# Kernel optimization log

Hardware: AMD Instinct MI355X
Metric: run time of the kernel (lower is better)

The kernel has to match this reference:

```python
import jax, jax.numpy as jnp
import numpy as np

N_SKU, N_WH, N_SUP = 100000, 5000, 2000
D_IN, D_OUT, H = 128, 64, 4
DH = D_OUT // H  # 16
E_INTRA, E_CROSS = 400000, 200000
EPS_LN = 1e-5


def setup_inputs() -> dict:
    key = jax.random.key(0)
    ks = jax.random.split(key, 40)
    f32 = jnp.float32

    def edges(k, E, n_src, n_dst):
        k1, k2 = jax.random.split(k)
        return jnp.stack([
            jax.random.randint(k1, (E,), 0, n_src),
            jax.random.randint(k2, (E,), 0, n_dst),
        ]).astype(jnp.int32)

    inp = {
        'x_sku': jax.random.normal(ks[0], (N_SKU, D_IN), f32),
        'x_wh': jax.random.normal(ks[1], (N_WH, D_IN), f32),
        'x_sup': jax.random.normal(ks[2], (N_SUP, D_IN), f32),
    }
    names = ['plant', 'pg', 'sg', 'st', 'ship', 'supply']
    for i, nm in enumerate(names):
        inp['W_' + nm] = jax.random.normal(ks[3 + 2 * i], (D_IN, D_OUT), f32) * 0.05
        inp['a_' + nm] = jax.random.normal(ks[4 + 2 * i], (2 * DH,), f32) * 0.05
    inp['proj_W'] = jax.random.normal(ks[20], (2 * D_OUT, D_OUT), f32) * 0.05
    inp['proj_b'] = jnp.zeros((D_OUT,), f32)
    inp['ln_g'] = jnp.ones((D_OUT,), f32)
    inp['ln_b'] = jnp.zeros((D_OUT,), f32)
    inp['res_W'] = jax.random.normal(ks[21], (D_IN, D_OUT), f32) * 0.05
    inp['ei_plant'] = edges(ks[22], E_INTRA, N_SKU, N_SKU)
    inp['ei_pg'] = edges(ks[23], E_INTRA, N_SKU, N_SKU)
    inp['ei_sg'] = edges(ks[24], E_INTRA, N_SKU, N_SKU)
    inp['ei_st'] = edges(ks[25], E_INTRA, N_SKU, N_SKU)
    inp['ei_ship'] = edges(ks[26], E_CROSS, N_SKU, N_WH)
    inp['ei_supply'] = edges(ks[27], E_CROSS, N_SKU, N_SUP)
    return inp


def _gat_conv(src_feat, dst_feat, ei, W, a, num_dst):
    """One-edge-type multi-head GAT: ELU edge scores, per-dst softmax, scatter-add."""
    src_i, dst_i = ei[0], ei[1]
    h_src = (src_feat @ W).reshape(-1, H, DH)  # [N_src, H, dh]
    h_dst = (dst_feat @ W).reshape(-1, H, DH)  # [N_dst, H, dh]
    hs = h_src[src_i]  # [E, H, dh] gather
    hd = h_dst[dst_i]  # [E, H, dh]
    # a^T [h_src || h_dst], shared attention vector across heads
    e = jax.nn.elu(hs @ a[:DH] + hd @ a[DH:])  # [E, H]
    # numerically stable scatter-softmax over edges grouped by dst node
    e_max = jax.lax.stop_gradient(jax.ops.segment_max(e, dst_i, num_segments=num_dst))
    e_max = jnp.where(jnp.isfinite(e_max), e_max, 0.0)
    exp_e = jnp.exp(e - e_max[dst_i])
    denom = jax.ops.segment_sum(exp_e, dst_i, num_segments=num_dst)
    alpha = exp_e / (denom[dst_i] + 1e-12)  # [E, H]
    out = jax.ops.segment_sum(alpha[..., None] * hs, dst_i, num_segments=num_dst)
    return out.reshape(num_dst, D_OUT)


def reference(x_sku, x_wh, x_sup,
              W_plant, a_plant, W_pg, a_pg, W_sg, a_sg, W_st, a_st,
              W_ship, a_ship, W_supply, a_supply,
              proj_W, proj_b, ln_g, ln_b, res_W,
              ei_plant, ei_pg, ei_sg, ei_st, ei_ship, ei_supply):
    # branch A (intra sku->sku edge types), summed into sku accumulator
    oa_sku = (_gat_conv(x_sku, x_sku, ei_plant, W_plant, a_plant, N_SKU)
              + _gat_conv(x_sku, x_sku, ei_pg, W_pg, a_pg, N_SKU)
              + _gat_conv(x_sku, x_sku, ei_sg, W_sg, a_sg, N_SKU)
              + _gat_conv(x_sku, x_sku, ei_st, W_st, a_st, N_SKU))
    ob_sku = jnp.zeros((N_SKU, D_OUT), x_sku.dtype)
    # branch B (cross edge types)
    oa_wh = jnp.zeros((N_WH, D_OUT), x_wh.dtype)
    ob_wh = _gat_conv(x_sku, x_wh, ei_ship, W_ship, a_ship, N_WH)
    oa_sup = jnp.zeros((N_SUP, D_OUT), x_sup.dtype)
    ob_sup = _gat_conv(x_sku, x_sup, ei_supply, W_supply, a_supply, N_SUP)

    def finish(x, oa, ob):
        y = jnp.concatenate([oa, ob], axis=-1) @ proj_W + proj_b + x @ res_W
        mu = y.mean(-1, keepdims=True)
        var = ((y - mu) ** 2).mean(-1, keepdims=True)
        return (y - mu) / jnp.sqrt(var + EPS_LN) * ln_g + ln_b

    return (finish(x_sku, oa_sku, ob_sku),
            finish(x_wh, oa_wh, ob_wh),
            finish(x_sup, oa_sup, ob_sup))
```

## Files before the change

kernel.cpp:

```cpp
#include <hip/hip_runtime.h>
#include <hip/hip_bf16.h>
#include <cstdint>

#define NS 100000
#define NW 5000
#define NPS 2000
#define DI 128
#define DO 64
#define NSTRIPS (NS/16)
#define NFLAT (4*NS + NW + NPS)
#define NWPAD 5008
#define NBUK 134
#define BCAP 20480
#define CHUNK 8192

typedef unsigned short bfu;
typedef __attribute__((ext_vector_type(8))) short s8v;
typedef __attribute__((ext_vector_type(4))) float f4v;

__device__ inline bfu f2bf(float f) {
  uint32_t u = __float_as_uint(f);
  u = (u + 0x7FFFu + ((u >> 16) & 1u)) >> 16;
  return (bfu)u;
}
__device__ inline float bf2f(bfu u) {
  return __uint_as_float((uint32_t)u << 16);
}

__global__ void k_convert3(const float* __restrict__ x0, bfu* __restrict__ o0, int n0,
                           const float* __restrict__ x1, bfu* __restrict__ o1, int n1,
                           const float* __restrict__ x2, bfu* __restrict__ o2, int n2) {
  int t = blockIdx.x * 256 + threadIdx.x;
  const float* x; bfu* o; int i;
  if (t < n0) { x = x0; o = o0; i = t; }
  else if (t < n0 + n1) { x = x1; o = o1; i = t - n0; }
  else if (t < n0 + n1 + n2) { x = x2; o = o2; i = t - n0 - n1; }
  else return;
  const float4* p = (const float4*)x + (size_t)i * 2;
  float4 a = p[0], b = p[1];
  uint4 v;
  v.x = (uint32_t)f2bf(a.x) | ((uint32_t)f2bf(a.y) << 16);
  v.y = (uint32_t)f2bf(a.z) | ((uint32_t)f2bf(a.w) << 16);
  v.z = (uint32_t)f2bf(b.x) | ((uint32_t)f2bf(b.y) << 16);
  v.w = (uint32_t)f2bf(b.z) | ((uint32_t)f2bf(b.w) << 16);
  ((uint4*)o)[i] = v;
}

struct PackArgs {
  const float* W[6]; const float* a[6];
  const float* resW; const float* projW;
  bfu* Bp; bfu* Rp; bfu* Pp;
  float* wv_wh; float* wv_sup;
};
__global__ void k_pack_all(PackArgs P) {
  int t = blockIdx.x * 256 + threadIdx.x;
  if (t < 61440) {
    int ty = t / 10240, rem = t % 10240;
    int r = rem / 128, k = rem % 128;
    const float* W = P.W[ty]; const float* a = P.a[ty];
    float v = 0.f;
    if (r < 64) v = W[k * 64 + r];
    else if (r < 72) {
      int h = (r - 64) & 3;
      const float* av = (r < 68) ? a : (a + 16);
      #pragma unroll
      for (int m = 0; m < 16; ++m) v += W[k * 64 + h * 16 + m] * av[m];
    }
    P.Bp[ty * 10240 + rem] = f2bf(v);
  } else if (t < 69632) {
    int i = t - 61440; int j = i / 128, k = i % 128;
    P.Rp[i] = f2bf(P.resW[k * 64 + j]);
  } else if (t < 77824) {
    int i = t - 69632; int j = i / 128, k = i % 128;
    P.Pp[i] = f2bf(P.projW[k * 64 + j]);
  } else if (t < 78848) {
    int i = t - 77824; int which = i / 512;
    int k = (i % 512) / 4, h = i % 4;
    const float* W = P.W[4 + which]; const float* a = P.a[4 + which];
    float v = 0.f;
    #pragma unroll
    for (int m = 0; m < 16; ++m) v += W[k * 64 + h * 16 + m] * a[16 + m];
    (which ? P.wv_sup : P.wv_wh)[k * 4 + h] = v;
  }
}

__global__ __launch_bounds__(256, 2) void k_gemm2t(const bfu* __restrict__ xb,
    const bfu* __restrict__ Bp0, const bfu* __restrict__ Bp1,
    bfu* __restrict__ hb0, bfu* __restrict__ hb1,
    float* __restrict__ ss0, float* __restrict__ ss1,
    float* __restrict__ sd0, float* __restrict__ sd1, int nstrips) {
  int lane = threadIdx.x & 63;
  int l15 = lane & 15, q = lane >> 4;
  int w  = (int)((blockIdx.x * blockDim.x + threadIdx.x) >> 6);
  int nw = (int)((gridDim.x * blockDim.x) >> 6);
  s8v bfr[10][4];
  #pragma unroll
  for (int nt = 0; nt < 5; ++nt)
    #pragma unroll
    for (int kq = 0; kq < 4; ++kq) {
      bfr[nt][kq]     = *(const s8v*)(Bp0 + (size_t)(nt * 16 + l15) * 128 + kq * 32 + q * 8);
      bfr[5 + nt][kq] = *(const s8v*)(Bp1 + (size_t)(nt * 16 + l15) * 128 + kq * 32 + q * 8);
    }
  for (int s = w; s < nstrips; s += nw) {
    int mb = s * 16;
    f4v acc[10];
    #pragma unroll
    for (int u = 0; u < 10; ++u) acc[u] = (f4v){0.f, 0.f, 0.f, 0.f};
    const bfu* ar = xb + (size_t)(mb + l15) * 128 + q * 8;
    #pragma unroll
    for (int kq = 0; kq < 4; ++kq) {
      s8v af = *(const s8v*)(ar + kq * 32);
      #pragma unroll
      for (int u = 0; u < 10; ++u)
        acc[u] = __builtin_amdgcn_mfma_f32_16x16x32_bf16(af, bfr[u][kq], acc[u], 0, 0, 0);
    }
    #pragma unroll
    for (int u = 0; u < 10; ++u) {
      int nt = (u < 5) ? u : u - 5;
      bfu* hb = (u < 5) ? hb0 : hb1;
      float* ssrc = (u < 5) ? ss0 : ss1;
      float* sdst = (u < 5) ? sd0 : sd1;
      int c = nt * 16 + l15;
      #pragma unroll
      for (int r = 0; r < 4; ++r) {
        int node = mb + q * 4 + r;
        float v = acc[u][r];
        if (c < 64)      hb[(size_t)node * 64 + c] = f2bf(v);
        else if (c < 68) ssrc[(size_t)node * 4 + (c - 64)] = v;
        else if (c < 72) sdst[(size_t)node * 4 + (c - 68)] = v;
      }
    }
  }
}

__global__ __launch_bounds__(256) void k_scores(const float* __restrict__ x,
    const float* __restrict__ wv, float* __restrict__ sdst, int N) {
  int lane = threadIdx.x & 63;
  int w  = (int)((blockIdx.x * 256 + threadIdx.x) >> 6);
  int nw = (int)((gridDim.x * 256) >> 6);
  float4 wa = ((const float4*)wv)[lane];
  float4 wb = ((const float4*)wv)[64 + lane];
  for (int n = w; n < N; n += nw) {
    float xa = x[(size_t)n * 128 + lane], xc = x[(size_t)n * 128 + 64 + lane];
    float4 a;
    a.x = xa * wa.x + xc * wb.x; a.y = xa * wa.y + xc * wb.y;
    a.z = xa * wa.z + xc * wb.z; a.w = xa * wa.w + xc * wb.w;
    #pragma unroll
    for (int m = 1; m < 64; m <<= 1) {
      a.x += __shfl_xor(a.x, m); a.y += __shfl_xor(a.y, m);
      a.z += __shfl_xor(a.z, m); a.w += __shfl_xor(a.w, m);
    }
    if (lane == 0) ((float4*)sdst)[n] = a;
  }
}

struct ESeg { const int* ei[6]; int E[6]; int Ecum[7]; };

__device__ inline void buk_of(int t, int d, int& b, int& loc) {
  if (t < 4)       { int f = d * 4 + t; b = f >> 12;        loc = f & 4095; }
  else if (t == 4) { b = 98 + (d >> 8);                     loc = d & 255; }
  else             { b = 118 + (d >> 7);                    loc = d & 127; }
}

__global__ void k_init_cur(int* __restrict__ gCur) {
  int t = threadIdx.x;
  if (t < NBUK) gCur[t] = t * BCAP;
}

__global__ __launch_bounds__(256) void k_bin(ESeg S, int* __restrict__ gCur,
                                             uint32_t* __restrict__ binned, int ETOT) {
  __shared__ int cnt[NBUK];
  __shared__ int runb[NBUK];
  int tid = threadIdx.x;
  int gbase = blockIdx.x * CHUNK;
  if (tid < NBUK) cnt[tid] = 0;
  __syncthreads();
  #pragma unroll 4
  for (int i = 0; i < CHUNK / 256; ++i) {
    int g = gbase + i * 256 + tid;
    if (g < ETOT) {
      int t = 0;
      #pragma unroll
      for (int k = 0; k < 5; ++k) t += (g >= S.Ecum[k + 1]);
      int e = g - S.Ecum[t];
      int d = S.ei[t][S.E[t] + e];
      int b, loc; buk_of(t, d, b, loc);
      atomicAdd(&cnt[b], 1);
    }
  }
  __syncthreads();
  if (tid < NBUK) { runb[tid] = atomicAdd(&gCur[tid], cnt[tid]); cnt[tid] = 0; }
  __syncthreads();
  #pragma unroll 4
  for (int i = 0; i < CHUNK / 256; ++i) {
    int g = gbase + i * 256 + tid;
    if (g < ETOT) {
      int t = 0;
      #pragma unroll
      for (int k = 0; k < 5; ++k) t += (g >= S.Ecum[k + 1]);
      int e = g - S.Ecum[t];
      int sv = S.ei[t][e];
      int d  = S.ei[t][S.E[t] + e];
      int b, loc; buk_of(t, d, b, loc);
      int pos = runb[b] + atomicAdd(&cnt[b], 1);
      if (pos < (b + 1) * BCAP)
        binned[pos] = ((uint32_t)loc << 17) | (uint32_t)sv;
    }
  }
}

__global__ __launch_bounds__(1024) void k_csr(const int* __restrict__ gCur,
    const uint32_t* __restrict__ binned, int* __restrict__ offs,
    int* __restrict__ ssorted) {
  __shared__ int hist[4096];
  __shared__ int wsc[16];
  __shared__ int bbase_s, cnt_s;
  int b = blockIdx.x, tid = threadIdx.x;
  int lane = tid & 63, wid = tid >> 6;
  if (tid == 0) {
    int bb = 0, own = 0;
    for (int k = 0; k < NBUK; ++k) {
      int c = min(gCur[k] - k * BCAP, BCAP);
      if (k < b) bb += c;
      if (k == b) own = c;
    }
    bbase_s = bb; cnt_s = own;
  }
  #pragma unroll
  for (int k = 0; k < 4; ++k) hist[tid * 4 + k] = 0;
  __syncthreads();
  int cnt = cnt_s, bbase = bbase_s;
  const uint32_t* bk = binned + (size_t)b * BCAP;
  for (int i = tid; i < cnt; i += 1024)
    atomicAdd(&hist[bk[i] >> 17], 1);
  __syncthreads();
  int t4 = tid * 4;
  int v0 = hist[t4], v1 = hist[t4 + 1], v2 = hist[t4 + 2], v3 = hist[t4 + 3];
  int tsum = v0 + v1 + v2 + v3;
  int inc = tsum;
  #pragma unroll
  for (int d = 1; d < 64; d <<= 1) { int tt = __shfl_up(inc, d); if (lane >= d) inc += tt; }
  if (lane == 63) wsc[wid] = inc;
  __syncthreads();
  int wpre = 0;
  for (int k = 0; k < wid; ++k) wpre += wsc[k];
  int excl = inc - tsum + wpre;
  hist[t4] = excl;
  hist[t4 + 1] = excl + v0;
  hist[t4 + 2] = excl + v0 + v1;
  hist[t4 + 3] = excl + v0 + v1 + v2;
  __syncthreads();
  int sbase, nslots;
  if (b < 98)        { sbase = b << 12;                nslots = min(4096, 4 * NS - sbase); }
  else if (b < 118)  { int lb = (b - 98) << 8;  sbase = 4 * NS + lb;      nslots = min(256, NW - lb); }
  else               { int lb = (b - 118) << 7; sbase = 4 * NS + NW + lb; nslots = min(128, NPS - lb); }
  for (int i = tid; i < nslots; i += 1024) offs[sbase + i] = bbase + hist[i];
  if (b == NBUK - 1 && tid == 0) offs[NFLAT] = bbase + cnt;
  __syncthreads();
  for (int i = tid; i < cnt; i += 1024) {
    uint32_t v = bk[i];
    int p = atomicAdd(&hist[v >> 17], 1);
    ssorted[bbase + p] = (int)(v & 0x1FFFFu);
  }
}

struct AggArgs {
  const int* offs; const int* srcs;
  const bfu* hbAll;
  const float* ssAll;
  const float* sdAll;
  const float* sd_wh; const float* sd_sup;
  bfu* osku; bfu* owh; bfu* osup;
};

__global__ __launch_bounds__(256) void k_megaagg(AggArgs A) {
  int lane = threadIdx.x & 63;
  int q = lane >> 4, m = lane & 15, h = m >> 2;
  int qsh = q << 4;
  int w  = (int)((blockIdx.x * 256 + threadIdx.x) >> 6);
  int nw = (int)((gridDim.x * 256) >> 6);
  for (int n = w; n < NS + NW + NPS; n += nw) {
    if (n < NS) {
      const int* ob = A.offs + (size_t)n * 4;
      int4 o = *(const int4*)ob;
      int o4 = ob[4];
      int sb = (q == 0) ? o.x : (q == 1) ? o.y : (q == 2) ? o.z : o.w;
      int se = (q == 0) ? o.y : (q == 1) ? o.z : (q == 2) ? o.w : o4;
      int len = se - sb;
      int maxlen = max(max(o.y - o.x, o.z - o.y), max(o.w - o.z, o4 - o.w));
      float sdv = A.sdAll[((size_t)q * NS + n) * 4 + h];
      uint32_t tbase = (uint32_t)q * (uint32_t)NS;
      float den = 0.f, a0 = 0.f, a1 = 0.f, a2 = 0.f, a3 = 0.f;
      for (int j0 = 0; j0 < maxlen; j0 += 16) {
        int ei = j0 + m;
        int sidx = (ei < len) ? A.srcs[sb + ei] : 0;
        int gmax = min(16, maxlen - j0);
        for (int jj = 0; jj < gmax; jj += 8) {
          float sc[8]; uint2 hv[8]; int vj[8];
          #pragma unroll
          for (int i = 0; i < 8; ++i) {
            int j = jj + i;
            int s = __shfl(sidx, qsh + j);
            vj[i] = (j0 + j) < len;
            uint32_t nb = tbase + (uint32_t)s;
            sc[i] = A.ssAll[nb * 4u + (uint32_t)h];
            hv[i] = *(const uint2*)(A.hbAll + nb * 64u + (uint32_t)(m * 4));
          }
          #pragma unroll
          for (int i = 0; i < 8; ++i) {
            float e = sc[i] + sdv;
            e = e > 0.f ? e : (__expf(e) - 1.f);
            float wgt = vj[i] ? __expf(e) : 0.f;
            den += wgt;
            a0 = fmaf(__uint_as_float(hv[i].x << 16), wgt, a0);
            a1 = fmaf(__uint_as_float(hv[i].x & 0xffff0000u), wgt, a1);
            a2 = fmaf(__uint_as_float(hv[i].y << 16), wgt, a2);
            a3 = fmaf(__uint_as_float(hv[i].y & 0xffff0000u), wgt, a3);
          }
        }
      }
      float inv = __builtin_amdgcn_rcpf(den + 1e-12f);
      float r0 = a0 * inv, r1 = a1 * inv, r2 = a2 * inv, r3 = a3 * inv;
      r0 += __shfl_xor(r0, 16); r0 += __shfl_xor(r0, 32);
      r1 += __shfl_xor(r1, 16); r1 += __shfl_xor(r1, 32);
      r2 += __shfl_xor(r2, 16); r2 += __shfl_xor(r2, 32);
      r3 += __shfl_xor(r3, 16); r3 += __shfl_xor(r3, 32);
      if (q == 0) {
        uint2 pk;
        pk.x = (uint32_t)f2bf(r0) | ((uint32_t)f2bf(r1) << 16);
        pk.y = (uint32_t)f2bf(r2) | ((uint32_t)f2bf(r3) << 16);
        *(uint2*)(A.osku + (size_t)n * 64 + m * 4) = pk;
      }
    } else {
      int tt, nl; const float* sd; bfu* op;
      int fi;
      if (n < NS + NW) { tt = 4; nl = n - NS; fi = 4 * NS + nl; sd = A.sd_wh; op = A.owh + (size_t)nl * 64; }
      else { tt = 5; nl = n - NS - NW; fi = 4 * NS + NW + nl; sd = A.sd_sup; op = A.osup + (size_t)nl * 64; }
      int beg = A.offs[fi], end = A.offs[fi + 1];
      uint32_t tbase = (uint32_t)tt * (uint32_t)NS;
      float sdv = sd[(size_t)nl * 4 + h];
      float den = 0.f, a0 = 0.f, a1 = 0.f, a2 = 0.f, a3 = 0.f;
      for (int cb = beg; cb < end; cb += 64) {
        int rem = min(64, end - cb);
        int sidx = (lane < rem) ? A.srcs[cb + lane] : 0;
        for (int jb = 0; jb < rem; jb += 32) {
          float sc[8]; uint2 hv[8]; int vj[8];
          #pragma unroll
          for (int i = 0; i < 8; ++i) {
            int eidx = jb + 4 * i + q;
            int s = __shfl(sidx, eidx);
            vj[i] = eidx < rem;
            uint32_t nb = tbase + (uint32_t)s;
            sc[i] = A.ssAll[nb * 4u + (uint32_t)h];
            hv[i] = *(const uint2*)(A.hbAll + nb * 64u + (uint32_t)(m * 4));
          }
          #pragma unroll
          for (int i = 0; i < 8; ++i) {
            float e = sc[i] + sdv;
            e = e > 0.f ? e : (__expf(e) - 1.f);
            float wgt = vj[i] ? __expf(e) : 0.f;
            den += wgt;
            a0 = fmaf(__uint_as_float(hv[i].x << 16), wgt, a0);
            a1 = fmaf(__uint_as_float(hv[i].x & 0xffff0000u), wgt, a1);
            a2 = fmaf(__uint_as_float(hv[i].y << 16), wgt, a2);
            a3 = fmaf(__uint_as_float(hv[i].y & 0xffff0000u), wgt, a3);
          }
        }
      }
      den += __shfl_xor(den, 16); den += __shfl_xor(den, 32);
      a0 += __shfl_xor(a0, 16); a0 += __shfl_xor(a0, 32);
      a1 += __shfl_xor(a1, 16); a1 += __shfl_xor(a1, 32);
      a2 += __shfl_xor(a2, 16); a2 += __shfl_xor(a2, 32);
      a3 += __shfl_xor(a3, 16); a3 += __shfl_xor(a3, 32);
      float inv = __builtin_amdgcn_rcpf(den + 1e-12f);
      if (q == 0) {
        uint2 pk;
        pk.x = (uint32_t)f2bf(a0 * inv) | ((uint32_t)f2bf(a1 * inv) << 16);
        pk.y = (uint32_t)f2bf(a2 * inv) | ((uint32_t)f2bf(a3 * inv) << 16);
        *(uint2*)(op + m * 4) = pk;
      }
    }
  }
}

__global__ __launch_bounds__(256) void k_finishM(const bfu* __restrict__ aggb,
    const bfu* __restrict__ xbf, const bfu* __restrict__ Pp, int koff,
    const bfu* __restrict__ Rp, const float* __restrict__ pb,
    const float* __restrict__ g, const float* __restrict__ bb,
    float* __restrict__ outp, int N, int nstrips) {
  int lane = threadIdx.x & 63, l15 = lane & 15, q = lane >> 4;
  int w  = (int)((blockIdx.x * 256 + threadIdx.x) >> 6);
  int nw = (int)((gridDim.x * 256) >> 6);
  s8v bP[4][2], bR[4][4];
  float pbv[4], gv[4], bv[4];
  #pragma unroll
  for (int c = 0; c < 4; ++c) {
    const bfu* pr = Pp + (size_t)(c * 16 + l15) * 128 + koff;
    bP[c][0] = *(const s8v*)(pr + q * 8);
    bP[c][1] = *(const s8v*)(pr + 32 + q * 8);
    const bfu* rr = Rp + (size_t)(c * 16 + l15) * 128;
    #pragma unroll
    for (int kq = 0; kq < 4; ++kq) bR[c][kq] = *(const s8v*)(rr + kq * 32 + q * 8);
    pbv[c] = pb[c * 16 + l15]; gv[c] = g[c * 16 + l15]; bv[c] = bb[c * 16 + l15];
  }
  for (int s = w; s < nstrips; s += nw) {
    int mb = s * 16;
    const bfu* ar = aggb + (size_t)(mb + l15) * 64 + q * 8;
    const bfu* xr = xbf + (size_t)(mb + l15) * 128 + q * 8;
    s8v a0 = *(const s8v*)ar, a1 = *(const s8v*)(ar + 32);
    s8v x0 = *(const s8v*)xr, x1 = *(const s8v*)(xr + 32),
        x2 = *(const s8v*)(xr + 64), x3 = *(const s8v*)(xr + 96);
    f4v acc[4];
    #pragma unroll
    for (int c = 0; c < 4; ++c) {
      acc[c] = (f4v){0.f, 0.f, 0.f, 0.f};
      acc[c] = __builtin_amdgcn_mfma_f32_16x16x32_bf16(a0, bP[c][0], acc[c], 0, 0, 0);
      acc[c] = __builtin_amdgcn_mfma_f32_16x16x32_bf16(a1, bP[c][1], acc[c], 0, 0, 0);
      acc[c] = __builtin_amdgcn_mfma_f32_16x16x32_bf16(x0, bR[c][0], acc[c], 0, 0, 0);
      acc[c] = __builtin_amdgcn_mfma_f32_16x16x32_bf16(x1, bR[c][1], acc[c], 0, 0, 0);
      acc[c] = __builtin_amdgcn_mfma_f32_16x16x32_bf16(x2, bR[c][2], acc[c], 0, 0, 0);
      acc[c] = __builtin_amdgcn_mfma_f32_16x16x32_bf16(x3, bR[c][3], acc[c], 0, 0, 0);
    }
    #pragma unroll
    for (int r = 0; r < 4; ++r) {
      int row = mb + q * 4 + r;
      float y0 = acc[0][r] + pbv[0], y1 = acc[1][r] + pbv[1];
      float y2 = acc[2][r] + pbv[2], y3 = acc[3][r] + pbv[3];
      float s1 = y0 + y1 + y2 + y3;
      s1 += __shfl_xor(s1, 1); s1 += __shfl_xor(s1, 2);
      s1 += __shfl_xor(s1, 4); s1 += __shfl_xor(s1, 8);
      float mu = s1 * 0.015625f;
      float d0 = y0 - mu, d1 = y1 - mu, d2 = y2 - mu, d3 = y3 - mu;
      float s2 = d0 * d0 + d1 * d1 + d2 * d2 + d3 * d3;
      s2 += __shfl_xor(s2, 1); s2 += __shfl_xor(s2, 2);
      s2 += __shfl_xor(s2, 4); s2 += __shfl_xor(s2, 8);
      float rs = rsqrtf(s2 * 0.015625f + 1e-5f);
      if (row < N) {
        float* orow = outp + (size_t)row * 64 + l15;
        orow[0]  = d0 * rs * gv[0] + bv[0];
        orow[16] = d1 * rs * gv[1] + bv[1];
        orow[32] = d2 * rs * gv[2] + bv[2];
        orow[48] = d3 * rs * gv[3] + bv[3];
      }
    }
  }
}

extern "C" void kernel_launch(void* const* d_in, const int* in_sizes, int n_in,
                              void* d_out, int out_size, void* d_ws, size_t ws_size,
                              hipStream_t stream) {
  const float* x_sku = (const float*)d_in[0];
  const float* x_wh  = (const float*)d_in[1];
  const float* x_sup = (const float*)d_in[2];
  const float* Wt[6]; const float* at[6];
  for (int t = 0; t < 6; ++t) { Wt[t] = (const float*)d_in[3 + 2 * t]; at[t] = (const float*)d_in[4 + 2 * t]; }
  const float* projW = (const float*)d_in[15];
  const float* projb = (const float*)d_in[16];
  const float* lng   = (const float*)d_in[17];
  const float* lnb   = (const float*)d_in[18];
  const float* resW  = (const float*)d_in[19];
  const int* ei[6]; int Et[6];
  for (int t = 0; t < 6; ++t) { ei[t] = (const int*)d_in[20 + t]; Et[t] = in_sizes[20 + t] / 2; }
  float* out = (float*)d_out;

  int ETOT = 0;
  for (int t = 0; t < 6; ++t) ETOT += Et[t];

  char* ws = (char*)d_ws;
  size_t off = 0;
  auto alloc = [&](size_t bytes) { off = (off + 255) & ~(size_t)255; void* p = ws + off; off += bytes; return p; };

  bfu*  xb      = (bfu*)alloc((size_t)NS * DI * 2);
  bfu*  xb_wh   = (bfu*)alloc((size_t)NWPAD * DI * 2);
  bfu*  xb_sup  = (bfu*)alloc((size_t)NPS * DI * 2);
  bfu*  Bp      = (bfu*)alloc((size_t)6 * 80 * 128 * 2);
  bfu*  Rp      = (bfu*)alloc((size_t)64 * 128 * 2);
  bfu*  Pp      = (bfu*)alloc((size_t)64 * 128 * 2);
  float* wv_wh  = (float*)alloc(128 * 4 * 4);
  float* wv_sup = (float*)alloc(128 * 4 * 4);
  bfu*  hbAll   = (bfu*)alloc((size_t)6 * NS * 64 * 2);
  float* ssAll  = (float*)alloc((size_t)6 * NS * 4 * 4);
  float* sdAll  = (float*)alloc((size_t)6 * NS * 4 * 4);
  float* sdst_wh  = (float*)alloc((size_t)NW * 4 * 4);
  float* sdst_sup = (float*)alloc((size_t)NPS * 4 * 4);
  size_t agg_bytes = ((size_t)NS + NWPAD + NPS) * 64 * 2;
  size_t bin_bytes = (size_t)NBUK * BCAP * 4;
  char* un = (char*)alloc(agg_bytes > bin_bytes ? agg_bytes : bin_bytes);
  bfu* agg_sku = (bfu*)un;
  bfu* agg_wh  = agg_sku + (size_t)NS * 64;
  bfu* agg_sup = agg_wh + (size_t)NWPAD * 64;
  uint32_t* binned = (uint32_t*)un;
  int* gCur    = (int*)alloc(256 * 4);
  int* offsb   = (int*)alloc((size_t)(NFLAT + 1) * 4);
  int* ssorted = (int*)alloc((size_t)ETOT * 4);

  int n0 = NS * 16, n1 = NW * 16, n2 = NPS * 16;
  k_convert3<<<(n0 + n1 + n2 + 255) / 256, 256, 0, stream>>>(x_sku, xb, n0, x_wh, xb_wh, n1,
                                                             x_sup, xb_sup, n2);

  PackArgs PA;
  for (int t = 0; t < 6; ++t) { PA.W[t] = Wt[t]; PA.a[t] = at[t]; }
  PA.resW = resW; PA.projW = projW; PA.Bp = Bp; PA.Rp = Rp; PA.Pp = Pp;
  PA.wv_wh = wv_wh; PA.wv_sup = wv_sup;
  k_pack_all<<<(78848 + 255) / 256, 256, 0, stream>>>(PA);

  k_scores<<<1250, 256, 0, stream>>>(x_wh, wv_wh, sdst_wh, NW);
  k_scores<<<500, 256, 0, stream>>>(x_sup, wv_sup, sdst_sup, NPS);

  ESeg S;
  S.Ecum[0] = 0;
  for (int t = 0; t < 6; ++t) { S.ei[t] = ei[t]; S.E[t] = Et[t]; S.Ecum[t + 1] = S.Ecum[t] + Et[t]; }
  k_init_cur<<<1, 256, 0, stream>>>(gCur);
  k_bin<<<(ETOT + CHUNK - 1) / CHUNK, 256, 0, stream>>>(S, gCur, binned, ETOT);
  k_csr<<<NBUK, 1024, 0, stream>>>(gCur, binned, offsb, ssorted);

  for (int p = 0; p < 3; ++p) {
    int t0 = 2 * p, t1 = 2 * p + 1;
    k_gemm2t<<<512, 256, 0, stream>>>(xb, Bp + (size_t)t0 * 10240, Bp + (size_t)t1 * 10240,
        hbAll + (size_t)t0 * NS * 64, hbAll + (size_t)t1 * NS * 64,
        ssAll + (size_t)t0 * NS * 4, ssAll + (size_t)t1 * NS * 4,
        sdAll + (size_t)t0 * NS * 4, sdAll + (size_t)t1 * NS * 4, NSTRIPS);
  }

  AggArgs A;
  A.offs = offsb; A.srcs = ssorted;
  A.hbAll = hbAll; A.ssAll = ssAll; A.sdAll = sdAll;
  A.sd_wh = sdst_wh; A.sd_sup = sdst_sup;
  A.osku = agg_sku; A.owh = agg_wh; A.osup = agg_sup;
  k_megaagg<<<(NS + NW + NPS + 3) / 4, 256, 0, stream>>>(A);

  k_finishM<<<1563, 256, 0, stream>>>(agg_sku, xb, Pp, 0, Rp, projb, lng, lnb, out, NS, NSTRIPS);
  k_finishM<<<79, 256, 0, stream>>>(agg_wh, xb_wh, Pp, 64, Rp, projb, lng, lnb,
                                    out + (size_t)NS * 64, NW, NWPAD / 16);
  k_finishM<<<32, 256, 0, stream>>>(agg_sup, xb_sup, Pp, 64, Rp, projb, lng, lnb,
                                    out + (size_t)(NS + NW) * 64, NPS, NPS / 16);
}
```

Measured before the change: 416.1 us.

## Merge front-end, GEMM and finish launches into fewer multi-role kernels

Folds the convert, pack, scores, init and bin kernels into one block-role-dispatched front kernel, the three GEMM launches into one 1536-block grid, and the three finish launches into one. The scores kernel now computes its attention-weight vectors inline instead of reading a precomputed buffer, and bin cursors become per-bucket local offsets cleared with a memset. The aim is to cut launch overhead and inter-kernel gaps by letting independent stages run concurrently. The cost is extra per-block dispatch logic and shared-memory use sized for the largest role in the merged kernel.

```diff
diff --git a/kernel.cpp b/kernel.cpp
--- a/kernel.cpp
+++ b/kernel.cpp
@@ -14,6 +14,11 @@
 #define BCAP 20480
 #define CHUNK 8192
 
+#define B_CONV 6688
+#define B_PACK 304
+#define B_SWH  157
+#define B_SSUP 63
+
 typedef unsigned short bfu;
 typedef __attribute__((ext_vector_type(8))) short s8v;
 typedef __attribute__((ext_vector_type(4))) float f4v;
@@ -27,14 +32,77 @@
   return __uint_as_float((uint32_t)u << 16);
 }
 
-__global__ void k_convert3(const float* __restrict__ x0, bfu* __restrict__ o0, int n0,
-                           const float* __restrict__ x1, bfu* __restrict__ o1, int n1,
-                           const float* __restrict__ x2, bfu* __restrict__ o2, int n2) {
-  int t = blockIdx.x * 256 + threadIdx.x;
+struct ESeg { const int* ei[6]; int E[6]; int Ecum[7]; };
+
+__device__ inline void buk_of(int t, int d, int& b, int& loc) {
+  if (t < 4)       { int f = d * 4 + t; b = f >> 12;        loc = f & 4095; }
+  else if (t == 4) { b = 98 + (d >> 8);                     loc = d & 255; }
+  else             { b = 118 + (d >> 7);                    loc = d & 127; }
+}
+
+struct PackA {
+  const float* W[6]; const float* a[6];
+  const float* resW; const float* projW;
+  bfu* Bp; bfu* Rp; bfu* Pp;
+};
+
+struct K1Args {
+  ESeg S; int* gCur; uint32_t* binned; int ETOT; int nbin;
+  const float* x0; bfu* o0; int n0;
+  const float* x1; bfu* o1; int n1;
+  const float* x2; bfu* o2; int n2;
+  PackA P;
+  const float* xwh; const float* xsup; float* sd_wh; float* sd_sup;
+};
+
+__device__ void bin_body(const K1Args& A, int bid) {
+  __shared__ int cnt[NBUK];
+  __shared__ int runb[NBUK];
+  const ESeg& S = A.S;
+  int tid = threadIdx.x;
+  int gbase = bid * CHUNK;
+  if (tid < NBUK) cnt[tid] = 0;
+  __syncthreads();
+  #pragma unroll 4
+  for (int i = 0; i < CHUNK / 256; ++i) {
+    int g = gbase + i * 256 + tid;
+    if (g < A.ETOT) {
+      int t = 0;
+      #pragma unroll
+      for (int k = 0; k < 5; ++k) t += (g >= S.Ecum[k + 1]);
+      int e = g - S.Ecum[t];
+      int d = S.ei[t][S.E[t] + e];
+      int b, loc; buk_of(t, d, b, loc);
+      atomicAdd(&cnt[b], 1);
+    }
+  }
+  __syncthreads();
+  if (tid < NBUK) { runb[tid] = atomicAdd(&A.gCur[tid], cnt[tid]); cnt[tid] = 0; }
+  __syncthreads();
+  #pragma unroll 4
+  for (int i = 0; i < CHUNK / 256; ++i) {
+    int g = gbase + i * 256 + tid;
+    if (g < A.ETOT) {
+      int t = 0;
+      #pragma unroll
+      for (int k = 0; k < 5; ++k) t += (g >= S.Ecum[k + 1]);
+      int e = g - S.Ecum[t];
+      int sv = S.ei[t][e];
+      int d  = S.ei[t][S.E[t] + e];
+      int b, loc; buk_of(t, d, b, loc);
+      int pos = runb[b] + atomicAdd(&cnt[b], 1);
+      if (pos < BCAP)
+        A.binned[(size_t)b * BCAP + pos] = ((uint32_t)loc << 17) | (uint32_t)sv;
+    }
+  }
+}
+
+__device__ void convert_body(const K1Args& A, int bid) {
+  int t = bid * 256 + threadIdx.x;
   const float* x; bfu* o; int i;
-  if (t < n0) { x = x0; o = o0; i = t; }
-  else if (t < n0 + n1) { x = x1; o = o1; i = t - n0; }
-  else if (t < n0 + n1 + n2) { x = x2; o = o2; i = t - n0 - n1; }
+  if (t < A.n0) { x = A.x0; o = A.o0; i = t; }
+  else if (t < A.n0 + A.n1) { x = A.x1; o = A.o1; i = t - A.n0; }
+  else if (t < A.n0 + A.n1 + A.n2) { x = A.x2; o = A.o2; i = t - A.n0 - A.n1; }
   else return;
   const float4* p = (const float4*)x + (size_t)i * 2;
   float4 a = p[0], b = p[1];
@@ -46,14 +114,8 @@
   ((uint4*)o)[i] = v;
 }
 
-struct PackArgs {
-  const float* W[6]; const float* a[6];
-  const float* resW; const float* projW;
-  bfu* Bp; bfu* Rp; bfu* Pp;
-  float* wv_wh; float* wv_sup;
-};
-__global__ void k_pack_all(PackArgs P) {
-  int t = blockIdx.x * 256 + threadIdx.x;
+__device__ void pack_body(const PackA& P, int bid) {
+  int t = bid * 256 + threadIdx.x;
   if (t < 61440) {
     int ty = t / 10240, rem = t % 10240;
     int r = rem / 128, k = rem % 128;
@@ -73,26 +135,126 @@
   } else if (t < 77824) {
     int i = t - 69632; int j = i / 128, k = i % 128;
     P.Pp[i] = f2bf(P.projW[k * 64 + j]);
-  } else if (t < 78848) {
-    int i = t - 77824; int which = i / 512;
-    int k = (i % 512) / 4, h = i % 4;
-    const float* W = P.W[4 + which]; const float* a = P.a[4 + which];
-    float v = 0.f;
-    #pragma unroll
-    for (int m = 0; m < 16; ++m) v += W[k * 64 + h * 16 + m] * a[16 + m];
-    (which ? P.wv_sup : P.wv_wh)[k * 4 + h] = v;
-  }
-}
-
-__global__ __launch_bounds__(256, 2) void k_gemm2t(const bfu* __restrict__ xb,
-    const bfu* __restrict__ Bp0, const bfu* __restrict__ Bp1,
-    bfu* __restrict__ hb0, bfu* __restrict__ hb1,
-    float* __restrict__ ss0, float* __restrict__ ss1,
-    float* __restrict__ sd0, float* __restrict__ sd1, int nstrips) {
+  }
+}
+
+__device__ void scores_body(const float* __restrict__ x, const float* __restrict__ W,
+                            const float* __restrict__ a, float* __restrict__ sdst,
+                            int N, int bid, int nblk) {
+  int tid = threadIdx.x;
+  int lane = tid & 63;
+  float wa[4] = {0.f, 0.f, 0.f, 0.f}, wb[4] = {0.f, 0.f, 0.f, 0.f};
+  for (int m = 0; m < 16; ++m) {
+    float av = a[16 + m];
+    #pragma unroll
+    for (int h = 0; h < 4; ++h) {
+      wa[h] += W[lane * 64 + h * 16 + m] * av;
+      wb[h] += W[(64 + lane) * 64 + h * 16 + m] * av;
+    }
+  }
+  int w  = (bid * 256 + tid) >> 6;
+  int nw = (nblk * 256) >> 6;
+  for (int n = w; n < N; n += nw) {
+    float xa = x[(size_t)n * 128 + lane], xc = x[(size_t)n * 128 + 64 + lane];
+    float4 r;
+    r.x = xa * wa[0] + xc * wb[0]; r.y = xa * wa[1] + xc * wb[1];
+    r.z = xa * wa[2] + xc * wb[2]; r.w = xa * wa[3] + xc * wb[3];
+    #pragma unroll
+    for (int m = 1; m < 64; m <<= 1) {
+      r.x += __shfl_xor(r.x, m); r.y += __shfl_xor(r.y, m);
+      r.z += __shfl_xor(r.z, m); r.w += __shfl_xor(r.w, m);
+    }
+    if (lane == 0) ((float4*)sdst)[n] = r;
+  }
+}
+
+__global__ __launch_bounds__(256) void k_front(K1Args A) {
+  int bid = blockIdx.x;
+  if (bid < A.nbin) { bin_body(A, bid); return; }
+  bid -= A.nbin;
+  if (bid < B_CONV) { convert_body(A, bid); return; }
+  bid -= B_CONV;
+  if (bid < B_PACK) { pack_body(A.P, bid); return; }
+  bid -= B_PACK;
+  if (bid < B_SWH) { scores_body(A.xwh, A.P.W[4], A.P.a[4], A.sd_wh, NW, bid, B_SWH); return; }
+  bid -= B_SWH;
+  scores_body(A.xsup, A.P.W[5], A.P.a[5], A.sd_sup, NPS, bid, B_SSUP);
+}
+
+__global__ __launch_bounds__(1024) void k_csr(const int* __restrict__ gCur,
+    const uint32_t* __restrict__ binned, int* __restrict__ offs,
+    int* __restrict__ ssorted) {
+  __shared__ int hist[4096];
+  __shared__ int wsc[16];
+  __shared__ int bbase_s, cnt_s;
+  int b = blockIdx.x, tid = threadIdx.x;
+  int lane = tid & 63, wid = tid >> 6;
+  if (tid == 0) {
+    int bb = 0, own = 0;
+    for (int k = 0; k < NBUK; ++k) {
+      int c = min(gCur[k], BCAP);
+      if (k < b) bb += c;
+      if (k == b) own = c;
+    }
+    bbase_s = bb; cnt_s = own;
+  }
+  #pragma unroll
+  for (int k = 0; k < 4; ++k) hist[tid * 4 + k] = 0;
+  __syncthreads();
+  int cnt = cnt_s, bbase = bbase_s;
+  const uint32_t* bk = binned + (size_t)b * BCAP;
+  for (int i = tid; i < cnt; i += 1024)
+    atomicAdd(&hist[bk[i] >> 17], 1);
+  __syncthreads();
+  int t4 = tid * 4;
+  int v0 = hist[t4], v1 = hist[t4 + 1], v2 = hist[t4 + 2], v3 = hist[t4 + 3];
+  int tsum = v0 + v1 + v2 + v3;
+  int inc = tsum;
+  #pragma unroll
+  for (int d = 1; d < 64; d <<= 1) { int tt = __shfl_up(inc, d); if (lane >= d) inc += tt; }
+  if (lane == 63) wsc[wid] = inc;
+  __syncthreads();
+  int wpre = 0;
+  for (int k = 0; k < wid; ++k) wpre += wsc[k];
+  int excl = inc - tsum + wpre;
+  hist[t4] = excl;
+  hist[t4 + 1] = excl + v0;
+  hist[t4 + 2] = excl + v0 + v1;
+  hist[t4 + 3] = excl + v0 + v1 + v2;
+  __syncthreads();
+  int sbase, nslots;
+  if (b < 98)        { sbase = b << 12;                nslots = min(4096, 4 * NS - sbase); }
+  else if (b < 118)  { int lb = (b - 98) << 8;  sbase = 4 * NS + lb;      nslots = min(256, NW - lb); }
+  else               { int lb = (b - 118) << 7; sbase = 4 * NS + NW + lb; nslots = min(128, NPS - lb); }
+  for (int i = tid; i < nslots; i += 1024) offs[sbase + i] = bbase + hist[i];
+  if (b == NBUK - 1 && tid == 0) offs[NFLAT] = bbase + cnt;
+  __syncthreads();
+  for (int i = tid; i < cnt; i += 1024) {
+    uint32_t v = bk[i];
+    int p = atomicAdd(&hist[v >> 17], 1);
+    ssorted[bbase + p] = (int)(v & 0x1FFFFu);
+  }
+}
+
+struct GemmArgs {
+  const bfu* xb; const bfu* Bp;
+  bfu* hbAll; float* ssAll; float* sdAll; int nstrips;
+};
+__global__ __launch_bounds__(256, 2) void k_gemm(GemmArgs G) {
+  int p = blockIdx.x >> 9;
+  int bloc = blockIdx.x & 511;
+  const bfu* Bp0 = G.Bp + (size_t)(2 * p) * 10240;
+  const bfu* Bp1 = G.Bp + (size_t)(2 * p + 1) * 10240;
+  bfu* hb0 = G.hbAll + (size_t)(2 * p) * NS * 64;
+  bfu* hb1 = G.hbAll + (size_t)(2 * p + 1) * NS * 64;
+  float* ss0 = G.ssAll + (size_t)(2 * p) * NS * 4;
+  float* ss1 = G.ssAll + (size_t)(2 * p + 1) * NS * 4;
+  float* sd0 = G.sdAll + (size_t)(2 * p) * NS * 4;
+  float* sd1 = G.sdAll + (size_t)(2 * p + 1) * NS * 4;
   int lane = threadIdx.x & 63;
   int l15 = lane & 15, q = lane >> 4;
-  int w  = (int)((blockIdx.x * blockDim.x + threadIdx.x) >> 6);
-  int nw = (int)((gridDim.x * blockDim.x) >> 6);
+  int w  = (int)((bloc * 256 + threadIdx.x) >> 6);
+  int nw = (512 * 256) >> 6;
   s8v bfr[10][4];
   #pragma unroll
   for (int nt = 0; nt < 5; ++nt)
@@ -101,12 +263,12 @@
       bfr[nt][kq]     = *(const s8v*)(Bp0 + (size_t)(nt * 16 + l15) * 128 + kq * 32 + q * 8);
       bfr[5 + nt][kq] = *(const s8v*)(Bp1 + (size_t)(nt * 16 + l15) * 128 + kq * 32 + q * 8);
     }
-  for (int s = w; s < nstrips; s += nw) {
+  for (int s = w; s < G.nstrips; s += nw) {
     int mb = s * 16;
     f4v acc[10];
     #pragma unroll
     for (int u = 0; u < 10; ++u) acc[u] = (f4v){0.f, 0.f, 0.f, 0.f};
-    const bfu* ar = xb + (size_t)(mb + l15) * 128 + q * 8;
+    const bfu* ar = G.xb + (size_t)(mb + l15) * 128 + q * 8;
     #pragma unroll
     for (int kq = 0; kq < 4; ++kq) {
       s8v af = *(const s8v*)(ar + kq * 32);
@@ -130,137 +292,6 @@
         else if (c < 72) sdst[(size_t)node * 4 + (c - 68)] = v;
       }
     }
-  }
-}
-
-__global__ __launch_bounds__(256) void k_scores(const float* __restrict__ x,
-    const float* __restrict__ wv, float* __restrict__ sdst, int N) {
-  int lane = threadIdx.x & 63;
-  int w  = (int)((blockIdx.x * 256 + threadIdx.x) >> 6);
-  int nw = (int)((gridDim.x * 256) >> 6);
-  float4 wa = ((const float4*)wv)[lane];
-  float4 wb = ((const float4*)wv)[64 + lane];
-  for (int n = w; n < N; n += nw) {
-    float xa = x[(size_t)n * 128 + lane], xc = x[(size_t)n * 128 + 64 + lane];
-    float4 a;
-    a.x = xa * wa.x + xc * wb.x; a.y = xa * wa.y + xc * wb.y;
-    a.z = xa * wa.z + xc * wb.z; a.w = xa * wa.w + xc * wb.w;
-    #pragma unroll
-    for (int m = 1; m < 64; m <<= 1) {
-      a.x += __shfl_xor(a.x, m); a.y += __shfl_xor(a.y, m);
-      a.z += __shfl_xor(a.z, m); a.w += __shfl_xor(a.w, m);
-    }
-    if (lane == 0) ((float4*)sdst)[n] = a;
-  }
-}
-
-struct ESeg { const int* ei[6]; int E[6]; int Ecum[7]; };
-
-__device__ inline void buk_of(int t, int d, int& b, int& loc) {
-  if (t < 4)       { int f = d * 4 + t; b = f >> 12;        loc = f & 4095; }
-  else if (t == 4) { b = 98 + (d >> 8);                     loc = d & 255; }
-  else             { b = 118 + (d >> 7);                    loc = d & 127; }
-}
-
-__global__ void k_init_cur(int* __restrict__ gCur) {
-  int t = threadIdx.x;
-  if (t < NBUK) gCur[t] = t * BCAP;
-}
-
-__global__ __launch_bounds__(256) void k_bin(ESeg S, int* __restrict__ gCur,
-                                             uint32_t* __restrict__ binned, int ETOT) {
-  __shared__ int cnt[NBUK];
-  __shared__ int runb[NBUK];
-  int tid = threadIdx.x;
-  int gbase = blockIdx.x * CHUNK;
-  if (tid < NBUK) cnt[tid] = 0;
-  __syncthreads();
-  #pragma unroll 4
-  for (int i = 0; i < CHUNK / 256; ++i) {
-    int g = gbase + i * 256 + tid;
-    if (g < ETOT) {
-      int t = 0;
-      #pragma unroll
-      for (int k = 0; k < 5; ++k) t += (g >= S.Ecum[k + 1]);
-      int e = g - S.Ecum[t];
-      int d = S.ei[t][S.E[t] + e];
-      int b, loc; buk_of(t, d, b, loc);
-      atomicAdd(&cnt[b], 1);
-    }
-  }
-  __syncthreads();
-  if (tid < NBUK) { runb[tid] = atomicAdd(&gCur[tid], cnt[tid]); cnt[tid] = 0; }
-  __syncthreads();
-  #pragma unroll 4
-  for (int i = 0; i < CHUNK / 256; ++i) {
-    int g = gbase + i * 256 + tid;
-    if (g < ETOT) {
-      int t = 0;
-      #pragma unroll
-      for (int k = 0; k < 5; ++k) t += (g >= S.Ecum[k + 1]);
-      int e = g - S.Ecum[t];
-      int sv = S.ei[t][e];
-      int d  = S.ei[t][S.E[t] + e];
-      int b, loc; buk_of(t, d, b, loc);
-      int pos = runb[b] + atomicAdd(&cnt[b], 1);
-      if (pos < (b + 1) * BCAP)
-        binned[pos] = ((uint32_t)loc << 17) | (uint32_t)sv;
-    }
-  }
-}
-
-__global__ __launch_bounds__(1024) void k_csr(const int* __restrict__ gCur,
-    const uint32_t* __restrict__ binned, int* __restrict__ offs,
-    int* __restrict__ ssorted) {
-  __shared__ int hist[4096];
-  __shared__ int wsc[16];
-  __shared__ int bbase_s, cnt_s;
-  int b = blockIdx.x, tid = threadIdx.x;
-  int lane = tid & 63, wid = tid >> 6;
-  if (tid == 0) {
-    int bb = 0, own = 0;
-    for (int k = 0; k < NBUK; ++k) {
-      int c = min(gCur[k] - k * BCAP, BCAP);
-      if (k < b) bb += c;
-      if (k == b) own = c;
-    }
-    bbase_s = bb; cnt_s = own;
-  }
-  #pragma unroll
-  for (int k = 0; k < 4; ++k) hist[tid * 4 + k] = 0;
-  __syncthreads();
-  int cnt = cnt_s, bbase = bbase_s;
-  const uint32_t* bk = binned + (size_t)b * BCAP;
-  for (int i = tid; i < cnt; i += 1024)
-    atomicAdd(&hist[bk[i] >> 17], 1);
-  __syncthreads();
-  int t4 = tid * 4;
-  int v0 = hist[t4], v1 = hist[t4 + 1], v2 = hist[t4 + 2], v3 = hist[t4 + 3];
-  int tsum = v0 + v1 + v2 + v3;
-  int inc = tsum;
-  #pragma unroll
-  for (int d = 1; d < 64; d <<= 1) { int tt = __shfl_up(inc, d); if (lane >= d) inc += tt; }
-  if (lane == 63) wsc[wid] = inc;
-  __syncthreads();
-  int wpre = 0;
-  for (int k = 0; k < wid; ++k) wpre += wsc[k];
-  int excl = inc - tsum + wpre;
-  hist[t4] = excl;
-  hist[t4 + 1] = excl + v0;
-  hist[t4 + 2] = excl + v0 + v1;
-  hist[t4 + 3] = excl + v0 + v1 + v2;
-  __syncthreads();
-  int sbase, nslots;
-  if (b < 98)        { sbase = b << 12;                nslots = min(4096, 4 * NS - sbase); }
-  else if (b < 118)  { int lb = (b - 98) << 8;  sbase = 4 * NS + lb;      nslots = min(256, NW - lb); }
-  else               { int lb = (b - 118) << 7; sbase = 4 * NS + NW + lb; nslots = min(128, NPS - lb); }
-  for (int i = tid; i < nslots; i += 1024) offs[sbase + i] = bbase + hist[i];
-  if (b == NBUK - 1 && tid == 0) offs[NFLAT] = bbase + cnt;
-  __syncthreads();
-  for (int i = tid; i < cnt; i += 1024) {
-    uint32_t v = bk[i];
-    int p = atomicAdd(&hist[v >> 17], 1);
-    ssorted[bbase + p] = (int)(v & 0x1FFFFu);
   }
 }
 
@@ -383,25 +414,42 @@
   }
 }
 
-__global__ __launch_bounds__(256) void k_finishM(const bfu* __restrict__ aggb,
-    const bfu* __restrict__ xbf, const bfu* __restrict__ Pp, int koff,
-    const bfu* __restrict__ Rp, const float* __restrict__ pb,
-    const float* __restrict__ g, const float* __restrict__ bb,
-    float* __restrict__ outp, int N, int nstrips) {
+struct FinArgs {
+  const bfu* agg0; const bfu* agg1; const bfu* agg2;
+  const bfu* x0; const bfu* x1; const bfu* x2;
+  float* out0; float* out1; float* out2;
+  const bfu* Pp; const bfu* Rp;
+  const float* pb; const float* g; const float* bb;
+  int bcut0, bcut1;
+};
+
+__global__ __launch_bounds__(256) void k_finish(FinArgs F) {
+  int bid = blockIdx.x;
+  int role = (bid >= F.bcut0) + (bid >= F.bcut1);
+  int b0 = (role == 0) ? 0 : (role == 1) ? F.bcut0 : F.bcut1;
+  int nb = (role == 0) ? F.bcut0 : (role == 1) ? (F.bcut1 - F.bcut0) : ((int)gridDim.x - F.bcut1);
+  int bloc = bid - b0;
+  const bfu* aggb = (role == 0) ? F.agg0 : (role == 1) ? F.agg1 : F.agg2;
+  const bfu* xbf  = (role == 0) ? F.x0 : (role == 1) ? F.x1 : F.x2;
+  float* outp     = (role == 0) ? F.out0 : (role == 1) ? F.out1 : F.out2;
+  int koff    = (role == 0) ? 0 : 64;
+  int N       = (role == 0) ? NS : (role == 1) ? NW : NPS;
+  int nstrips = (role == 0) ? NSTRIPS : (role == 1) ? (NWPAD / 16) : (NPS / 16);
+
   int lane = threadIdx.x & 63, l15 = lane & 15, q = lane >> 4;
-  int w  = (int)((blockIdx.x * 256 + threadIdx.x) >> 6);
-  int nw = (int)((gridDim.x * 256) >> 6);
+  int w  = (int)((bloc * 256 + threadIdx.x) >> 6);
+  int nw = nb << 2;
   s8v bP[4][2], bR[4][4];
   float pbv[4], gv[4], bv[4];
   #pragma unroll
   for (int c = 0; c < 4; ++c) {
-    const bfu* pr = Pp + (size_t)(c * 16 + l15) * 128 + koff;
+    const bfu* pr = F.Pp + (size_t)(c * 16 + l15) * 128 + koff;
     bP[c][0] = *(const s8v*)(pr + q * 8);
     bP[c][1] = *(const s8v*)(pr + 32 + q * 8);
-    const bfu* rr = Rp + (size_t)(c * 16 + l15) * 128;
+    const bfu* rr = F.Rp + (size_t)(c * 16 + l15) * 128;
     #pragma unroll
     for (int kq = 0; kq < 4; ++kq) bR[c][kq] = *(const s8v*)(rr + kq * 32 + q * 8);
-    pbv[c] = pb[c * 16 + l15]; gv[c] = g[c * 16 + l15]; bv[c] = bb[c * 16 + l15];
+    pbv[c] = F.pb[c * 16 + l15]; gv[c] = F.g[c * 16 + l15]; bv[c] = F.bb[c * 16 + l15];
   }
   for (int s = w; s < nstrips; s += nw) {
     int mb = s * 16;
@@ -476,8 +524,6 @@
   bfu*  Bp      = (bfu*)alloc((size_t)6 * 80 * 128 * 2);
   bfu*  Rp      = (bfu*)alloc((size_t)64 * 128 * 2);
   bfu*  Pp      = (bfu*)alloc((size_t)64 * 128 * 2);
-  float* wv_wh  = (float*)alloc(128 * 4 * 4);
-  float* wv_sup = (float*)alloc(128 * 4 * 4);
   bfu*  hbAll   = (bfu*)alloc((size_t)6 * NS * 64 * 2);
   float* ssAll  = (float*)alloc((size_t)6 * NS * 4 * 4);
   float* sdAll  = (float*)alloc((size_t)6 * NS * 4 * 4);
@@ -494,33 +540,27 @@
   int* offsb   = (int*)alloc((size_t)(NFLAT + 1) * 4);
   int* ssorted = (int*)alloc((size_t)ETOT * 4);
 
-  int n0 = NS * 16, n1 = NW * 16, n2 = NPS * 16;
-  k_convert3<<<(n0 + n1 + n2 + 255) / 256, 256, 0, stream>>>(x_sku, xb, n0, x_wh, xb_wh, n1,
-                                                             x_sup, xb_sup, n2);
-
-  PackArgs PA;
-  for (int t = 0; t < 6; ++t) { PA.W[t] = Wt[t]; PA.a[t] = at[t]; }
-  PA.resW = resW; PA.projW = projW; PA.Bp = Bp; PA.Rp = Rp; PA.Pp = Pp;
-  PA.wv_wh = wv_wh; PA.wv_sup = wv_sup;
-  k_pack_all<<<(78848 + 255) / 256, 256, 0, stream>>>(PA);
-
-  k_scores<<<1250, 256, 0, stream>>>(x_wh, wv_wh, sdst_wh, NW);
-  k_scores<<<500, 256, 0, stream>>>(x_sup, wv_sup, sdst_sup, NPS);
-
-  ESeg S;
-  S.Ecum[0] = 0;
-  for (int t = 0; t < 6; ++t) { S.ei[t] = ei[t]; S.E[t] = Et[t]; S.Ecum[t + 1] = S.Ecum[t] + Et[t]; }
-  k_init_cur<<<1, 256, 0, stream>>>(gCur);
-  k_bin<<<(ETOT + CHUNK - 1) / CHUNK, 256, 0, stream>>>(S, gCur, binned, ETOT);
+  hipMemsetAsync(gCur, 0, NBUK * 4, stream);
+
+  K1Args K;
+  K.S.Ecum[0] = 0;
+  for (int t = 0; t < 6; ++t) { K.S.ei[t] = ei[t]; K.S.E[t] = Et[t]; K.S.Ecum[t + 1] = K.S.Ecum[t] + Et[t]; }
+  K.gCur = gCur; K.binned = binned; K.ETOT = ETOT;
+  K.nbin = (ETOT + CHUNK - 1) / CHUNK;
+  K.x0 = x_sku; K.o0 = xb;     K.n0 = NS * 16;
+  K.x1 = x_wh;  K.o1 = xb_wh;  K.n1 = NW * 16;
+  K.x2 = x_sup; K.o2 = xb_sup; K.n2 = NPS * 16;
+  for (int t = 0; t < 6; ++t) { K.P.W[t] = Wt[t]; K.P.a[t] = at[t]; }
+  K.P.resW = resW; K.P.projW = projW; K.P.Bp = Bp; K.P.Rp = Rp; K.P.Pp = Pp;
+  K.xwh = x_wh; K.xsup = x_sup; K.sd_wh = sdst_wh; K.sd_sup = sdst_sup;
+  int gfront = K.nbin + B_CONV + B_PACK + B_SWH + B_SSUP;
+  k_front<<<gfront, 256, 0, stream>>>(K);
+
   k_csr<<<NBUK, 1024, 0, stream>>>(gCur, binned, offsb, ssorted);
 
-  for (int p = 0; p < 3; ++p) {
-    int t0 = 2 * p, t1 = 2 * p + 1;
-    k_gemm2t<<<512, 256, 0, stream>>>(xb, Bp + (size_t)t0 * 10240, Bp + (size_t)t1 * 10240,
-        hbAll + (size_t)t0 * NS * 64, hbAll + (size_t)t1 * NS * 64,
-        ssAll + (size_t)t0 * NS * 4, ssAll + (size_t)t1 * NS * 4,
-        sdAll + (size_t)t0 * NS * 4, sdAll + (size_t)t1 * NS * 4, NSTRIPS);
-  }
+  GemmArgs G;
+  G.xb = xb; G.Bp = Bp; G.hbAll = hbAll; G.ssAll = ssAll; G.sdAll = sdAll; G.nstrips = NSTRIPS;
+  k_gemm<<<1536, 256, 0, stream>>>(G);
 
   AggArgs A;
   A.offs = offsb; A.srcs = ssorted;
@@ -529,9 +569,11 @@
   A.osku = agg_sku; A.owh = agg_wh; A.osup = agg_sup;
   k_megaagg<<<(NS + NW + NPS + 3) / 4, 256, 0, stream>>>(A);
 
-  k_finishM<<<1563, 256, 0, stream>>>(agg_sku, xb, Pp, 0, Rp, projb, lng, lnb, out, NS, NSTRIPS);
-  k_finishM<<<79, 256, 0, stream>>>(agg_wh, xb_wh, Pp, 64, Rp, projb, lng, lnb,
-                                    out + (size_t)NS * 64, NW, NWPAD / 16);
-  k_finishM<<<32, 256, 0, stream>>>(agg_sup, xb_sup, Pp, 64, Rp, projb, lng, lnb,
-                                    out + (size_t)(NS + NW) * 64, NPS, NPS / 16);
-}
+  FinArgs F;
+  F.agg0 = agg_sku; F.agg1 = agg_wh; F.agg2 = agg_sup;
+  F.x0 = xb; F.x1 = xb_wh; F.x2 = xb_sup;
+  F.out0 = out; F.out1 = out + (size_t)NS * 64; F.out2 = out + (size_t)(NS + NW) * 64;
+  F.Pp = Pp; F.Rp = Rp; F.pb = projb; F.g = lng; F.bb = lnb;
+  F.bcut0 = 1563; F.bcut1 = 1563 + 79;
+  k_finish<<<1563 + 79 + 32, 256, 0, stream>>>(F);
+}
```

Result: faster. 378.8 us (-9.0%).
